# Kernel tuning notes

Measured on AMD Instinct MI355X. Metric: run time of the kernel, lower is better.

## Reference

```python
import jax, jax.numpy as jnp
import numpy as np

B, T, H, V = 64, 48, 512, 32000


def _uni(k, shape, fan_in):
    s = 1.0 / np.sqrt(fan_in)
    return jax.random.uniform(k, shape, jnp.float32, -s, s)


def setup_inputs() -> dict:
    key = jax.random.key(0)
    ks = jax.random.split(key, 21)
    inp = {
        "feat": jax.random.normal(ks[0], (B, T, H), jnp.float32),
        "caption": jax.random.normal(ks[1], (B, T, H), jnp.float32),
        "ids": jax.random.randint(ks[2], (B, T), 0, V),
    }
    i = 3
    for name, in_dim in (("1", H), ("2", 2 * H), ("d1", H), ("d2", 2 * H)):
        inp["w_ih" + name] = _uni(ks[i], (4 * H, in_dim), H); i += 1
        inp["w_hh" + name] = _uni(ks[i], (4 * H, H), H); i += 1
        inp["b_ih" + name] = _uni(ks[i], (4 * H,), H); i += 1
        inp["b_hh" + name] = _uni(ks[i], (4 * H,), H); i += 1
    inp["w_o"] = _uni(ks[i], (V, H), H); i += 1
    inp["b_o"] = _uni(ks[i], (V,), H)
    return inp


def lstm_cell(x, h, c, w_ih, w_hh, b_ih, b_hh):
    # PyTorch LSTMCell: gates in i, f, g, o order
    g = x @ w_ih.T + b_ih + h @ w_hh.T + b_hh
    gi, gf, gg, go = jnp.split(g, 4, axis=-1)
    c_new = jax.nn.sigmoid(gf) * c + jax.nn.sigmoid(gi) * jnp.tanh(gg)
    h_new = jax.nn.sigmoid(go) * jnp.tanh(c_new)
    return h_new, c_new


def reference(feat, caption, ids,
              w_ih1, w_hh1, b_ih1, b_hh1,
              w_ih2, w_hh2, b_ih2, b_hh2,
              w_ihd1, w_hhd1, b_ihd1, b_hhd1,
              w_ihd2, w_hhd2, b_ihd2, b_hhd2,
              w_o, b_o):
    pad = jnp.zeros((B, H), feat.dtype)
    z = jnp.zeros((B, H), feat.dtype)

    def enc_step(carry, x):
        h1, c1, h2, c2 = carry
        h1, c1 = lstm_cell(x, h1, c1, w_ih1, w_hh1, b_ih1, b_hh1)
        h2, c2 = lstm_cell(jnp.concatenate([pad, h1], 1), h2, c2,
                           w_ih2, w_hh2, b_ih2, b_hh2)
        return (h1, c1, h2, c2), None

    carry, _ = jax.lax.scan(enc_step, (z, z, z, z), jnp.swapaxes(feat, 0, 1))

    def dec_step(carry, xs):
        h1, c1, h2, c2 = carry
        cap, tgt = xs
        h1, c1 = lstm_cell(pad, h1, c1, w_ihd1, w_hhd1, b_ihd1, b_hhd1)
        h2, c2 = lstm_cell(jnp.concatenate([cap, h1], 1), h2, c2,
                           w_ihd2, w_hhd2, b_ihd2, b_hhd2)
        logits = h2 @ w_o.T + b_o  # [B, V]
        lp = jax.nn.log_softmax(logits, axis=-1)
        ce = -jnp.take_along_axis(lp, tgt[:, None], axis=1)[:, 0].mean()
        return (h1, c1, h2, c2), ce

    caps = jnp.swapaxes(caption[:, : T - 1, :], 0, 1)  # [T-1, B, H]
    tgts = jnp.swapaxes(ids[:, 1:T], 0, 1)             # [T-1, B]
    _, ces = jax.lax.scan(dec_step, carry, (caps, tgts))
    # total_loss += sum(mean_ce) / batch_size (word_loss is already a mean)
    return jnp.sum(ces) / B
```

## Files before the change

### kernel.cpp

```cpp
#include <hip/hip_runtime.h>
#include <math.h>

#define B_ 64
#define T_ 48
#define H_ 512
#define V_ 32000
#define G_ 2048
#define BH_ (B_*H_)
#define BG_ (B_*G_)

typedef short short8 __attribute__((ext_vector_type(8)));
typedef float f32x4 __attribute__((ext_vector_type(4)));

__device__ __forceinline__ float sigmoidf_(float x){ return 1.f/(1.f+__expf(-x)); }

__device__ __forceinline__ unsigned short f2bf(float f){
  unsigned u = __float_as_uint(f);
  u += 0x7fffu + ((u>>16)&1u);
  return (unsigned short)(u>>16);
}

__device__ __forceinline__ short8 cvt8(const float* g){
  float4 a = *(const float4*)g;
  float4 b = *(const float4*)(g+4);
  short8 v;
  v[0]=(short)f2bf(a.x); v[1]=(short)f2bf(a.y); v[2]=(short)f2bf(a.z); v[3]=(short)f2bf(a.w);
  v[4]=(short)f2bf(b.x); v[5]=(short)f2bf(b.y); v[6]=(short)f2bf(b.z); v[7]=(short)f2bf(b.w);
  return v;
}

__global__ void init_kernel(unsigned short* h1_0, unsigned short* h2_0, unsigned* flags){
  int i = blockIdx.x*256 + threadIdx.x;
  short8 z = {0,0,0,0,0,0,0,0};
  if (i < 4096) ((short8*)h1_0)[i] = z;
  else          ((short8*)h2_0)[i-4096] = z;
  if (i < 1152) flags[i] = 0u;
}

__global__ void cvt_cat_kernel(const float* __restrict__ s0, int ld0, int off0,
                               const float* __restrict__ s1, int ld1, int off1,
                               unsigned short* __restrict__ dst, int dld, long total8)
{
  int cols8 = dld >> 3;
  for (long i = blockIdx.x*256 + threadIdx.x; i < total8; i += (long)gridDim.x*256){
    int r = (int)(i / cols8);
    int k = (int)(i - (long)r*cols8) * 8;
    short8 v = (k < 512 || !s1) ? cvt8(s0 + (long)r*ld0 + off0 + k)
                                : cvt8(s1 + (long)r*ld1 + off1 + (k-512));
    *(short8*)(dst + (long)r*dld + k) = v;
  }
}

__global__ void bias_sum_kernel(const float* a1, const float* a2, float* o1,
                                const float* b1, const float* b2, float* o2){
  int n = blockIdx.x*256 + threadIdx.x;
  if (n < G_){ o1[n] = a1[n] + a2[n]; o2[n] = b1[n] + b2[n]; }
}

__global__ __launch_bounds__(512,1) void mm_pre_kernel(
    const float* __restrict__ A, int a_bstride,
    const unsigned short* __restrict__ Wbf,
    const float* __restrict__ bA, const float* __restrict__ bB,
    float* __restrict__ out)
{
  const int s = blockIdx.x, n0 = blockIdx.y*256;
  const int t = threadIdx.x, w = t>>6, l = t&63, ln = l&15, lk = l>>4;
  __shared__ short8 smA[64*64];
  __shared__ short8 smB[256*8];

  const float* af32 = A + (long)s*H_;

  f32x4 acc[4][2];
#pragma unroll
  for (int mf=0; mf<4; ++mf)
#pragma unroll
    for (int nf=0; nf<2; ++nf) acc[mf][nf] = (f32x4){0.f,0.f,0.f,0.f};

#pragma unroll
  for (int i=0;i<8;++i){ int e=i*4096+t*8; int m=e>>9, k=e&511;
    smA[m*64 + ((k>>3)^(m&7))] = cvt8(&af32[(long)m*a_bstride + k]); }

  for (int kc=0; kc<8; ++kc){
    __syncthreads();
#pragma unroll
    for (int i=0;i<4;++i){ int e=i*4096+t*8; int n=e>>6, k=e&63;
      smB[n*8 + ((k>>3)^(n&7))] = *(const short8*)(Wbf + (long)(n0+n)*512 + kc*64 + k); }
    __syncthreads();
#pragma unroll
    for (int ks2=0; ks2<2; ++ks2){
#pragma unroll
      for (int nf=0; nf<2; ++nf){
        int n = w*32 + nf*16 + ln;
        short8 bfr = smB[n*8 + ((ks2*4+lk)^(n&7))];
#pragma unroll
        for (int mf=0; mf<4; ++mf){
          int m = mf*16+ln;
          short8 afr = smA[m*64 + (((kc*2+ks2)*4+lk)^(m&7))];
          acc[mf][nf] = __builtin_amdgcn_mfma_f32_16x16x32_bf16(afr, bfr, acc[mf][nf], 0,0,0);
        }
      }
    }
  }
#pragma unroll
  for (int nf=0; nf<2; ++nf){
    int n = n0 + w*32 + nf*16 + ln;
    float bias = bA[n] + bB[n];
#pragma unroll
    for (int mf=0; mf<4; ++mf)
#pragma unroll
      for (int r=0; r<4; ++r){
        int m = mf*16 + lk*4 + r;
        out[(long)s*BG_ + (long)m*G_ + n] = acc[mf][nf][r] + bias;
      }
  }
}

__global__ __launch_bounds__(256,1) void fused_chain_kernel(
    const unsigned short* __restrict__ w1e, const unsigned short* __restrict__ w1d,
    const unsigned short* __restrict__ w2e, const unsigned short* __restrict__ w2d,
    const float* __restrict__ x1,
    const float* __restrict__ capq,
    const float* __restrict__ bd1s, const float* __restrict__ b2es,
    unsigned short* __restrict__ h1, unsigned short* __restrict__ h2,
    unsigned* __restrict__ flags)
{
  const int bc = blockIdx.x;
  const int isL2 = (bc >= 32);
  const int cb = bc & 31;
  const int t = threadIdx.x;
  const int wv = t>>6, l = t&63, ln = l&15, lk = l>>4;

  __shared__ short8 smA[64*128];
  __shared__ float gbuf[4][16][68];
  __shared__ float c_lds[16][68];
  unsigned short* stash = (unsigned short*)&smA[0];

  short8 W[32];
  const int col = wv*512 + cb*16 + ln;
  if (isL2){
    const long wrow = (long)col * 1024;
#pragma unroll
    for (int ks=0; ks<32; ++ks) W[ks] = *(const short8*)(w2e + wrow + ks*32 + lk*8);
  } else {
    const long wrow = (long)col * 512;
#pragma unroll
    for (int ks=0; ks<16; ++ks){
      W[ks]    = *(const short8*)(w1e + wrow + ks*32 + lk*8);
      W[16+ks] = *(const short8*)(w1d + wrow + ks*32 + lk*8);
    }
  }
  const float bext = isL2 ? b2es[col] : bd1s[col];

  for (int i=t; i<16*68; i+=256) (&c_lds[0][0])[i] = 0.f;

  for (int s=0; s<96; ++s){
    if (isL2 && s == 49){
      const long wrow = (long)col * 1024;
#pragma unroll
      for (int ks=0; ks<32; ++ks) W[ks] = *(const short8*)(w2d + wrow + ks*32 + lk*8);
    }
    const int active = isL2 ? (s>=1) : (s<95);
    if (active){
      if (!isL2){
        const unsigned short* hp = h1 + (long)s*BH_;
#pragma unroll
        for (int i=0;i<16;++i){ int e=i*2048+t*8; int m=e>>9, k=e&511;
          smA[m*128 + ((k>>3)^(m&7))] = *(const short8*)(hp + m*512 + k); }
      } else {
        const unsigned short* hpA = h2 + (long)(s-1)*BH_;
        const unsigned short* hpB = h1 + (long)s*BH_;
#pragma unroll
        for (int i=0;i<16;++i){ int e=i*2048+t*8; int m=e>>9, k=e&511;
          smA[m*128 + ((k>>3)^(m&7))]      = *(const short8*)(hpA + m*512 + k);
          smA[m*128 + ((k>>3)^(m&7)) + 64] = *(const short8*)(hpB + m*512 + k);
        }
      }

      const int dec = isL2 ? ((s-1)>=48) : (s>=48);
      float prev[4][4];
      if (!isL2){
        if (s < 48){
          const float* pp = x1 + (long)s*BG_ + col;
#pragma unroll
          for (int mf=0;mf<4;++mf)
#pragma unroll
            for (int r=0;r<4;++r) prev[mf][r] = pp[(long)(mf*16+lk*4+r)*G_];
        } else {
#pragma unroll
          for (int mf=0;mf<4;++mf)
#pragma unroll
            for (int r=0;r<4;++r) prev[mf][r] = bext;
        }
      } else {
        int s2 = s-1;
        if (s2 < 48){
#pragma unroll
          for (int mf=0;mf<4;++mf)
#pragma unroll
            for (int r=0;r<4;++r) prev[mf][r] = bext;
        } else {
          const float* pp = capq + (long)(s2-48)*BG_ + col;
#pragma unroll
          for (int mf=0;mf<4;++mf)
#pragma unroll
            for (int r=0;r<4;++r) prev[mf][r] = pp[(long)(mf*16+lk*4+r)*G_];
        }
      }
      __syncthreads();

      f32x4 acc[4];
#pragma unroll
      for (int mf=0;mf<4;++mf) acc[mf] = (f32x4){0.f,0.f,0.f,0.f};

      if (isL2){
#pragma unroll
        for (int ks=0; ks<32; ++ks)
#pragma unroll
          for (int mf=0; mf<4; ++mf){
            int m = mf*16+ln;
            acc[mf] = __builtin_amdgcn_mfma_f32_16x16x32_bf16(
              smA[m*128 + ((ks*4+lk)^(m&7))], W[ks], acc[mf], 0,0,0);
          }
      } else if (!dec){
#pragma unroll
        for (int ks=0; ks<16; ++ks)
#pragma unroll
          for (int mf=0; mf<4; ++mf){
            int m = mf*16+ln;
            acc[mf] = __builtin_amdgcn_mfma_f32_16x16x32_bf16(
              smA[m*128 + ((ks*4+lk)^(m&7))], W[ks], acc[mf], 0,0,0);
          }
      } else {
#pragma unroll
        for (int ks=0; ks<16; ++ks)
#pragma unroll
          for (int mf=0; mf<4; ++mf){
            int m = mf*16+ln;
            acc[mf] = __builtin_amdgcn_mfma_f32_16x16x32_bf16(
              smA[m*128 + ((ks*4+lk)^(m&7))], W[16+ks], acc[mf], 0,0,0);
          }
      }

#pragma unroll
      for (int mf=0;mf<4;++mf)
#pragma unroll
        for (int r=0;r<4;++r) acc[mf][r] += prev[mf][r];

#pragma unroll
      for (int mf=0;mf<4;++mf) *(f32x4*)&gbuf[wv][ln][mf*16+lk*4] = acc[mf];
      __syncthreads();

      {
        int n = t&15, m0 = (t>>4)*4;
        float4 gi = *(float4*)&gbuf[0][n][m0];
        float4 gf = *(float4*)&gbuf[1][n][m0];
        float4 gg = *(float4*)&gbuf[2][n][m0];
        float4 go = *(float4*)&gbuf[3][n][m0];
        float4 c4 = *(float4*)&c_lds[n][m0];
        float a_i[4]={gi.x,gi.y,gi.z,gi.w}, a_f[4]={gf.x,gf.y,gf.z,gf.w};
        float a_g[4]={gg.x,gg.y,gg.z,gg.w}, a_o[4]={go.x,go.y,go.z,go.w};
        float ci[4]={c4.x,c4.y,c4.z,c4.w};
        float cn[4];
#pragma unroll
        for (int j=0;j<4;++j){
          float i_ = sigmoidf_(a_i[j]), f_ = sigmoidf_(a_f[j]), o_ = sigmoidf_(a_o[j]);
          float g_ = tanhf(a_g[j]);
          cn[j] = f_*ci[j] + i_*g_;
          stash[(m0+j)*24 + n] = f2bf(o_*tanhf(cn[j]));
        }
        *(float4*)&c_lds[n][m0] = make_float4(cn[0],cn[1],cn[2],cn[3]);
      }
      __syncthreads();

      {
        unsigned short* ho = (isL2 ? (h2 + (long)s*BH_) : (h1 + (long)(s+1)*BH_)) + cb*16;
        int m = t>>2, q = t&3;
        unsigned long long v = *(const unsigned long long*)&stash[m*24 + q*4];
        __hip_atomic_store((unsigned long long*)(ho + (long)m*512 + q*4), v,
                           __ATOMIC_RELAXED, __HIP_MEMORY_SCOPE_AGENT);
      }
    }

    if (s < 95){
      unsigned g = (unsigned)(s+1);
      __syncthreads();
      if (t == 0)
        __hip_atomic_store(&flags[bc*16], g, __ATOMIC_RELAXED, __HIP_MEMORY_SCOPE_AGENT);
      if (t < 64){
        while (__hip_atomic_load(&flags[t*16], __ATOMIC_RELAXED, __HIP_MEMORY_SCOPE_AGENT) < g)
          __builtin_amdgcn_s_sleep(1);
      }
      __syncthreads();
    }
  }
}

__global__ __launch_bounds__(512,1) void ce_mfma_kernel(
    const unsigned short* __restrict__ h2_bf, const unsigned short* __restrict__ wo_bf,
    const float* __restrict__ b_o, const int* __restrict__ ids,
    float* __restrict__ partial, float* __restrict__ tgt)
{
  const int td = blockIdx.x, vt = blockIdx.y, v0 = vt*256;
  const int t = threadIdx.x, w = t>>6, l = t&63, ln = l&15, lk = l>>4;
  __shared__ short8 smA[64*64];
  __shared__ short8 smB[256*8];
  __shared__ float red[8][64];
  __shared__ int tid_s[64];

  const unsigned short* hp = h2_bf + (long)(49+td)*BH_;
  if (t < 64) tid_s[t] = ids[t*T_ + td + 1];
#pragma unroll
  for (int i=0;i<8;++i){ int e=i*4096+t*8; int m=e>>9, k=e&511;
    smA[m*64 + ((k>>3)^(m&7))] = *(const short8*)(hp + m*512 + k); }

  f32x4 acc[4][2];
#pragma unroll
  for (int mf=0; mf<4; ++mf)
#pragma unroll
    for (int nf=0; nf<2; ++nf) acc[mf][nf] = (f32x4){0.f,0.f,0.f,0.f};

  for (int kc=0; kc<8; ++kc){
    __syncthreads();
#pragma unroll
    for (int i=0;i<4;++i){ int e=i*4096+t*8; int n=e>>6, k=e&63;
      smB[n*8 + ((k>>3)^(n&7))] = *(const short8*)(wo_bf + (long)(v0+n)*512 + kc*64 + k); }
    __syncthreads();
#pragma unroll
    for (int ks2=0; ks2<2; ++ks2){
#pragma unroll
      for (int nf=0; nf<2; ++nf){
        int n = w*32 + nf*16 + ln;
        short8 bfr = smB[n*8 + ((ks2*4+lk)^(n&7))];
#pragma unroll
        for (int mf=0; mf<4; ++mf){
          int m = mf*16+ln;
          short8 afr = smA[m*64 + (((kc*2+ks2)*4+lk)^(m&7))];
          acc[mf][nf] = __builtin_amdgcn_mfma_f32_16x16x32_bf16(afr, bfr, acc[mf][nf], 0,0,0);
        }
      }
    }
  }

  float se[4][4];
#pragma unroll
  for (int mf=0; mf<4; ++mf)
#pragma unroll
    for (int r=0;r<4;++r) se[mf][r] = 0.f;
#pragma unroll
  for (int nf=0; nf<2; ++nf){
    int ng = v0 + w*32 + nf*16 + ln;
    float bo = b_o[ng];
#pragma unroll
    for (int mf=0; mf<4; ++mf)
#pragma unroll
      for (int r=0;r<4;++r){
        int m = mf*16 + lk*4 + r;
        float lg = acc[mf][nf][r] + bo;
        se[mf][r] += __expf(lg);
        if (ng == tid_s[m]) tgt[td*64 + m] = lg;
      }
  }
#pragma unroll
  for (int off=1; off<16; off<<=1)
#pragma unroll
    for (int mf=0; mf<4; ++mf)
#pragma unroll
      for (int r=0;r<4;++r) se[mf][r] += __shfl_xor(se[mf][r], off);
  if (ln == 0){
#pragma unroll
    for (int mf=0; mf<4; ++mf)
      *(f32x4*)&red[w][mf*16 + lk*4] = (f32x4){se[mf][0],se[mf][1],se[mf][2],se[mf][3]};
  }
  __syncthreads();
  if (t < 64){
    float ssum = 0.f;
#pragma unroll
    for (int w2=0; w2<8; ++w2) ssum += red[w2][t];
    partial[(long)vt*3008 + td*64 + t] = ssum;
  }
}

__global__ void ce_combine(const float* __restrict__ partial, const float* __restrict__ tgt,
                           float* __restrict__ ce_row){
  int r = blockIdx.x*256 + threadIdx.x;
  if (r < 3008){
    float s = 0.f;
    for (int i=0;i<125;++i) s += partial[(long)i*3008 + r];
    ce_row[r] = __logf(s) - tgt[r];
  }
}

__global__ void ce_final(const float* __restrict__ ce_row, float* __restrict__ out){
  __shared__ float red[256];
  float s = 0.f;
  for (int i=threadIdx.x; i<3008; i+=256) s += ce_row[i];
  red[threadIdx.x] = s;
  __syncthreads();
  for (int off=128; off>0; off>>=1){
    if (threadIdx.x < off) red[threadIdx.x] += red[threadIdx.x + off];
    __syncthreads();
  }
  if (threadIdx.x == 0) out[0] = red[0] * (1.0f/4096.0f);
}

extern "C" void kernel_launch(void* const* d_in, const int* in_sizes, int n_in,
                              void* d_out, int out_size, void* d_ws, size_t ws_size,
                              hipStream_t stream)
{
  (void)in_sizes; (void)n_in; (void)out_size; (void)ws_size;
  const float* feat    = (const float*)d_in[0];
  const float* caption = (const float*)d_in[1];
  const int*   ids     = (const int*)d_in[2];
  const float* w_ih1  = (const float*)d_in[3];
  const float* w_hh1  = (const float*)d_in[4];
  const float* b_ih1  = (const float*)d_in[5];
  const float* b_hh1  = (const float*)d_in[6];
  const float* w_ih2  = (const float*)d_in[7];
  const float* w_hh2  = (const float*)d_in[8];
  const float* b_ih2  = (const float*)d_in[9];
  const float* b_hh2  = (const float*)d_in[10];
  const float* w_hhd1 = (const float*)d_in[12];
  const float* b_ihd1 = (const float*)d_in[13];
  const float* b_hhd1 = (const float*)d_in[14];
  const float* w_ihd2 = (const float*)d_in[15];
  const float* w_hhd2 = (const float*)d_in[16];
  const float* b_ihd2 = (const float*)d_in[17];
  const float* b_hhd2 = (const float*)d_in[18];
  const float* w_o    = (const float*)d_in[19];
  const float* b_o    = (const float*)d_in[20];

  char* p = (char*)d_ws;
  unsigned short* h1   = (unsigned short*)p; p += 96L*BH_*2;
  unsigned short* h2   = (unsigned short*)p; p += 96L*BH_*2;
  unsigned short* w1e  = (unsigned short*)p; p += 2048L*512*2;
  unsigned short* w1d  = (unsigned short*)p; p += 2048L*512*2;
  unsigned short* w2e  = (unsigned short*)p; p += 2048L*1024*2;
  unsigned short* w2d  = (unsigned short*)p; p += 2048L*1024*2;
  unsigned short* wx1  = (unsigned short*)p; p += 2048L*512*2;
  unsigned short* wcap = (unsigned short*)p; p += 2048L*512*2;
  float* x1    = (float*)p;
  unsigned short* wo_bf = (unsigned short*)p;
  p += 48L*BG_*4;
  float* capq  = (float*)p; p += 47L*BG_*4;
  float* bd1s  = (float*)p; p += 2048*4;
  float* b2es  = (float*)p; p += 2048*4;
  float* partial = (float*)p; p += 125L*3008*4;
  float* tgt   = (float*)p; p += 3008*4;
  float* ce_row= (float*)p; p += 3008*4;
  unsigned* flags = (unsigned*)p; p += 1152*4;

  init_kernel<<<32, 256, 0, stream>>>(h1, h2, flags);

  cvt_cat_kernel<<<256, 256, 0, stream>>>(w_hh1, 512, 0, nullptr, 0, 0, w1e, 512, 2048L*64);
  cvt_cat_kernel<<<256, 256, 0, stream>>>(w_hhd1, 512, 0, nullptr, 0, 0, w1d, 512, 2048L*64);
  cvt_cat_kernel<<<256, 256, 0, stream>>>(w_hh2, 512, 0, w_ih2, 1024, 512, w2e, 1024, 2048L*128);
  cvt_cat_kernel<<<256, 256, 0, stream>>>(w_hhd2, 512, 0, w_ihd2, 1024, 512, w2d, 1024, 2048L*128);
  cvt_cat_kernel<<<256, 256, 0, stream>>>(w_ih1, 512, 0, nullptr, 0, 0, wx1, 512, 2048L*64);
  cvt_cat_kernel<<<256, 256, 0, stream>>>(w_ihd2, 1024, 0, nullptr, 0, 0, wcap, 512, 2048L*64);
  bias_sum_kernel<<<8, 256, 0, stream>>>(b_ihd1, b_hhd1, bd1s, b_ih2, b_hh2, b2es);

  mm_pre_kernel<<<dim3(48,8), 512, 0, stream>>>(feat, T_*H_, wx1, b_ih1, b_hh1, x1);
  mm_pre_kernel<<<dim3(47,8), 512, 0, stream>>>(caption, T_*H_, wcap, b_ihd2, b_hhd2, capq);

  fused_chain_kernel<<<64, 256, 0, stream>>>(w1e, w1d, w2e, w2d, x1, capq, bd1s, b2es, h1, h2, flags);

  cvt_cat_kernel<<<512, 256, 0, stream>>>(w_o, 512, 0, nullptr, 0, 0, wo_bf, 512, 32000L*64);

  ce_mfma_kernel<<<dim3(47,125), 512, 0, stream>>>(h2, wo_bf, b_o, ids, partial, tgt);
  ce_combine<<<12, 256, 0, stream>>>(partial, tgt, ce_row);
  ce_final<<<1, 256, 0, stream>>>(ce_row, (float*)d_out);
}
```

Baseline: 1.479 ms.

## Decouple layer-1 and layer-2 LSTM groups with separate counter barriers

Replaces the single 64-block all-to-all flag barrier with two independent 32-block counter/generation barriers, one per LSTM layer group. Layer-2 blocks now only wait on layer-1's generation counter, which lets layer 1 run ahead of layer 2 so the two chains pipeline instead of running in lockstep. Each barrier uses one atomic fetch_add and a single spinning thread instead of 64 threads polling 64 flags. The risks are contention on the shared counter and the need for the flags buffer to be zeroed and laid out for the new indices. Memory visibility relies only on relaxed atomics plus __syncthreads.

```diff
diff --git a/kernel.cpp b/kernel.cpp
--- a/kernel.cpp
+++ b/kernel.cpp
@@ -130,6 +130,11 @@
   const int t = threadIdx.x;
   const int wv = t>>6, l = t&63, ln = l&15, lk = l>>4;
 
+  unsigned* ctr1 = flags;
+  unsigned* gen1 = flags + 64;
+  unsigned* ctr2 = flags + 128;
+  unsigned* gen2 = flags + 192;
+
   __shared__ short8 smA[64*128];
   __shared__ float gbuf[4][16][68];
   __shared__ float c_lds[16][68];
@@ -152,76 +157,34 @@
   const float bext = isL2 ? b2es[col] : bd1s[col];
 
   for (int i=t; i<16*68; i+=256) (&c_lds[0][0])[i] = 0.f;
-
-  for (int s=0; s<96; ++s){
-    if (isL2 && s == 49){
-      const long wrow = (long)col * 1024;
-#pragma unroll
-      for (int ks=0; ks<32; ++ks) W[ks] = *(const short8*)(w2d + wrow + ks*32 + lk*8);
-    }
-    const int active = isL2 ? (s>=1) : (s<95);
-    if (active){
-      if (!isL2){
-        const unsigned short* hp = h1 + (long)s*BH_;
+  __syncthreads();
+
+  if (!isL2){
+    for (int u=0; u<95; ++u){
+      { const unsigned short* hp = h1 + (long)u*BH_;
 #pragma unroll
         for (int i=0;i<16;++i){ int e=i*2048+t*8; int m=e>>9, k=e&511;
-          smA[m*128 + ((k>>3)^(m&7))] = *(const short8*)(hp + m*512 + k); }
+          smA[m*128 + ((k>>3)^(m&7))] = *(const short8*)(hp + m*512 + k); } }
+
+      float prev[4][4];
+      if (u < 48){
+        const float* pp = x1 + (long)u*BG_ + col;
+#pragma unroll
+        for (int mf=0;mf<4;++mf)
+#pragma unroll
+          for (int r=0;r<4;++r) prev[mf][r] = pp[(long)(mf*16+lk*4+r)*G_];
       } else {
-        const unsigned short* hpA = h2 + (long)(s-1)*BH_;
-        const unsigned short* hpB = h1 + (long)s*BH_;
-#pragma unroll
-        for (int i=0;i<16;++i){ int e=i*2048+t*8; int m=e>>9, k=e&511;
-          smA[m*128 + ((k>>3)^(m&7))]      = *(const short8*)(hpA + m*512 + k);
-          smA[m*128 + ((k>>3)^(m&7)) + 64] = *(const short8*)(hpB + m*512 + k);
-        }
-      }
-
-      const int dec = isL2 ? ((s-1)>=48) : (s>=48);
-      float prev[4][4];
-      if (!isL2){
-        if (s < 48){
-          const float* pp = x1 + (long)s*BG_ + col;
-#pragma unroll
-          for (int mf=0;mf<4;++mf)
-#pragma unroll
-            for (int r=0;r<4;++r) prev[mf][r] = pp[(long)(mf*16+lk*4+r)*G_];
-        } else {
-#pragma unroll
-          for (int mf=0;mf<4;++mf)
-#pragma unroll
-            for (int r=0;r<4;++r) prev[mf][r] = bext;
-        }
-      } else {
-        int s2 = s-1;
-        if (s2 < 48){
-#pragma unroll
-          for (int mf=0;mf<4;++mf)
-#pragma unroll
-            for (int r=0;r<4;++r) prev[mf][r] = bext;
-        } else {
-          const float* pp = capq + (long)(s2-48)*BG_ + col;
-#pragma unroll
-          for (int mf=0;mf<4;++mf)
-#pragma unroll
-            for (int r=0;r<4;++r) prev[mf][r] = pp[(long)(mf*16+lk*4+r)*G_];
-        }
+#pragma unroll
+        for (int mf=0;mf<4;++mf)
+#pragma unroll
+          for (int r=0;r<4;++r) prev[mf][r] = bext;
       }
       __syncthreads();
 
       f32x4 acc[4];
 #pragma unroll
       for (int mf=0;mf<4;++mf) acc[mf] = (f32x4){0.f,0.f,0.f,0.f};
-
-      if (isL2){
-#pragma unroll
-        for (int ks=0; ks<32; ++ks)
-#pragma unroll
-          for (int mf=0; mf<4; ++mf){
-            int m = mf*16+ln;
-            acc[mf] = __builtin_amdgcn_mfma_f32_16x16x32_bf16(
-              smA[m*128 + ((ks*4+lk)^(m&7))], W[ks], acc[mf], 0,0,0);
-          }
-      } else if (!dec){
+      if (u < 48){
 #pragma unroll
         for (int ks=0; ks<16; ++ks)
 #pragma unroll
@@ -240,7 +203,6 @@
               smA[m*128 + ((ks*4+lk)^(m&7))], W[16+ks], acc[mf], 0,0,0);
           }
       }
-
 #pragma unroll
       for (int mf=0;mf<4;++mf)
 #pragma unroll
@@ -249,7 +211,6 @@
 #pragma unroll
       for (int mf=0;mf<4;++mf) *(f32x4*)&gbuf[wv][ln][mf*16+lk*4] = acc[mf];
       __syncthreads();
-
       {
         int n = t&15, m0 = (t>>4)*4;
         float4 gi = *(float4*)&gbuf[0][n][m0];
@@ -257,10 +218,10 @@
         float4 gg = *(float4*)&gbuf[2][n][m0];
         float4 go = *(float4*)&gbuf[3][n][m0];
         float4 c4 = *(float4*)&c_lds[n][m0];
+        float cn[4];
         float a_i[4]={gi.x,gi.y,gi.z,gi.w}, a_f[4]={gf.x,gf.y,gf.z,gf.w};
         float a_g[4]={gg.x,gg.y,gg.z,gg.w}, a_o[4]={go.x,go.y,go.z,go.w};
         float ci[4]={c4.x,c4.y,c4.z,c4.w};
-        float cn[4];
 #pragma unroll
         for (int j=0;j<4;++j){
           float i_ = sigmoidf_(a_i[j]), f_ = sigmoidf_(a_f[j]), o_ = sigmoidf_(a_o[j]);
@@ -271,26 +232,122 @@
         *(float4*)&c_lds[n][m0] = make_float4(cn[0],cn[1],cn[2],cn[3]);
       }
       __syncthreads();
-
       {
-        unsigned short* ho = (isL2 ? (h2 + (long)s*BH_) : (h1 + (long)(s+1)*BH_)) + cb*16;
+        unsigned short* ho = h1 + (long)(u+1)*BH_ + cb*16;
         int m = t>>2, q = t&3;
         unsigned long long v = *(const unsigned long long*)&stash[m*24 + q*4];
         __hip_atomic_store((unsigned long long*)(ho + (long)m*512 + q*4), v,
                            __ATOMIC_RELAXED, __HIP_MEMORY_SCOPE_AGENT);
       }
+      __syncthreads();
+      if (t == 0){
+        unsigned tgt = (unsigned)(u+1);
+        unsigned old = __hip_atomic_fetch_add(ctr1, 1u, __ATOMIC_RELAXED, __HIP_MEMORY_SCOPE_AGENT);
+        if (old == 32u*tgt - 1u)
+          __hip_atomic_store(gen1, tgt, __ATOMIC_RELAXED, __HIP_MEMORY_SCOPE_AGENT);
+        else
+          while (__hip_atomic_load(gen1, __ATOMIC_RELAXED, __HIP_MEMORY_SCOPE_AGENT) < tgt)
+            __builtin_amdgcn_s_sleep(1);
+      }
+      __syncthreads();
     }
-
-    if (s < 95){
-      unsigned g = (unsigned)(s+1);
-      __syncthreads();
-      if (t == 0)
-        __hip_atomic_store(&flags[bc*16], g, __ATOMIC_RELAXED, __HIP_MEMORY_SCOPE_AGENT);
-      if (t < 64){
-        while (__hip_atomic_load(&flags[t*16], __ATOMIC_RELAXED, __HIP_MEMORY_SCOPE_AGENT) < g)
+  } else {
+    for (int v=1; v<=95; ++v){
+      if (v == 49){
+        const long wrow = (long)col * 1024;
+#pragma unroll
+        for (int ks=0; ks<32; ++ks) W[ks] = *(const short8*)(w2d + wrow + ks*32 + lk*8);
+      }
+      if (t == 0){
+        while (__hip_atomic_load(gen1, __ATOMIC_RELAXED, __HIP_MEMORY_SCOPE_AGENT) < (unsigned)v)
           __builtin_amdgcn_s_sleep(1);
       }
       __syncthreads();
+
+      { const unsigned short* hpA = h2 + (long)(v-1)*BH_;
+        const unsigned short* hpB = h1 + (long)v*BH_;
+#pragma unroll
+        for (int i=0;i<16;++i){ int e=i*2048+t*8; int m=e>>9, k=e&511;
+          smA[m*128 + ((k>>3)^(m&7))]      = *(const short8*)(hpA + m*512 + k);
+          smA[m*128 + ((k>>3)^(m&7)) + 64] = *(const short8*)(hpB + m*512 + k);
+        } }
+
+      int s2 = v-1;
+      float prev[4][4];
+      if (s2 < 48){
+#pragma unroll
+        for (int mf=0;mf<4;++mf)
+#pragma unroll
+          for (int r=0;r<4;++r) prev[mf][r] = bext;
+      } else {
+        const float* pp = capq + (long)(s2-48)*BG_ + col;
+#pragma unroll
+        for (int mf=0;mf<4;++mf)
+#pragma unroll
+          for (int r=0;r<4;++r) prev[mf][r] = pp[(long)(mf*16+lk*4+r)*G_];
+      }
+      __syncthreads();
+
+      f32x4 acc[4];
+#pragma unroll
+      for (int mf=0;mf<4;++mf) acc[mf] = (f32x4){0.f,0.f,0.f,0.f};
+#pragma unroll
+      for (int ks=0; ks<32; ++ks)
+#pragma unroll
+        for (int mf=0; mf<4; ++mf){
+          int m = mf*16+ln;
+          acc[mf] = __builtin_amdgcn_mfma_f32_16x16x32_bf16(
+            smA[m*128 + ((ks*4+lk)^(m&7))], W[ks], acc[mf], 0,0,0);
+        }
+#pragma unroll
+      for (int mf=0;mf<4;++mf)
+#pragma unroll
+        for (int r=0;r<4;++r) acc[mf][r] += prev[mf][r];
+
+#pragma unroll
+      for (int mf=0;mf<4;++mf) *(f32x4*)&gbuf[wv][ln][mf*16+lk*4] = acc[mf];
+      __syncthreads();
+      {
+        int n = t&15, m0 = (t>>4)*4;
+        float4 gi = *(float4*)&gbuf[0][n][m0];
+        float4 gf = *(float4*)&gbuf[1][n][m0];
+        float4 gg = *(float4*)&gbuf[2][n][m0];
+        float4 go = *(float4*)&gbuf[3][n][m0];
+        float4 c4 = *(float4*)&c_lds[n][m0];
+        float cn[4];
+        float a_i[4]={gi.x,gi.y,gi.z,gi.w}, a_f[4]={gf.x,gf.y,gf.z,gf.w};
+        float a_g[4]={gg.x,gg.y,gg.z,gg.w}, a_o[4]={go.x,go.y,go.z,go.w};
+        float ci[4]={c4.x,c4.y,c4.z,c4.w};
+#pragma unroll
+        for (int j=0;j<4;++j){
+          float i_ = sigmoidf_(a_i[j]), f_ = sigmoidf_(a_f[j]), o_ = sigmoidf_(a_o[j]);
+          float g_ = tanhf(a_g[j]);
+          cn[j] = f_*ci[j] + i_*g_;
+          stash[(m0+j)*24 + n] = f2bf(o_*tanhf(cn[j]));
+        }
+        *(float4*)&c_lds[n][m0] = make_float4(cn[0],cn[1],cn[2],cn[3]);
+      }
+      __syncthreads();
+      {
+        unsigned short* ho = h2 + (long)v*BH_ + cb*16;
+        int m = t>>2, q = t&3;
+        unsigned long long vv = *(const unsigned long long*)&stash[m*24 + q*4];
+        __hip_atomic_store((unsigned long long*)(ho + (long)m*512 + q*4), vv,
+                           __ATOMIC_RELAXED, __HIP_MEMORY_SCOPE_AGENT);
+      }
+      __syncthreads();
+      if (v < 95){
+        if (t == 0){
+          unsigned tgt = (unsigned)v;
+          unsigned old = __hip_atomic_fetch_add(ctr2, 1u, __ATOMIC_RELAXED, __HIP_MEMORY_SCOPE_AGENT);
+          if (old == 32u*tgt - 1u)
+            __hip_atomic_store(gen2, tgt, __ATOMIC_RELAXED, __HIP_MEMORY_SCOPE_AGENT);
+          else
+            while (__hip_atomic_load(gen2, __ATOMIC_RELAXED, __HIP_MEMORY_SCOPE_AGENT) < tgt)
+              __builtin_amdgcn_s_sleep(1);
+        }
+        __syncthreads();
+      }
     }
   }
 }
```

Result: slower. 1.579 ms (+6.7%).

## Keep vocab tile resident in LDS across timesteps and store gate preacts as bf16

Applied to the files above, without the earlier changes.

The output-projection/CE kernel now launches one block per 128-wide vocab tile. Each block holds its bf16 w_o slice in shared memory and loops over all 47 decoder timesteps, streaming only the small h2 chunks. This replaces the 47x125 grid that reloaded w_o tiles from global memory for every timestep. Separately, the precomputed input-gate activations (x1, capq) are written and read as bf16 instead of fp32, halving that traffic in the serial chain kernel at some precision cost. The grid shrinks to 250 blocks with a serial timestep loop, which may limit parallelism.

```diff
diff --git a/kernel.cpp b/kernel.cpp
--- a/kernel.cpp
+++ b/kernel.cpp
@@ -18,6 +18,9 @@
   unsigned u = __float_as_uint(f);
   u += 0x7fffu + ((u>>16)&1u);
   return (unsigned short)(u>>16);
+}
+__device__ __forceinline__ float bf2f(unsigned short u){
+  return __uint_as_float(((unsigned)u)<<16);
 }
 
 __device__ __forceinline__ short8 cvt8(const float* g){
@@ -61,7 +64,7 @@
     const float* __restrict__ A, int a_bstride,
     const unsigned short* __restrict__ Wbf,
     const float* __restrict__ bA, const float* __restrict__ bB,
-    float* __restrict__ out)
+    unsigned short* __restrict__ out)
 {
   const int s = blockIdx.x, n0 = blockIdx.y*256;
   const int t = threadIdx.x, w = t>>6, l = t&63, ln = l&15, lk = l>>4;
@@ -110,7 +113,7 @@
 #pragma unroll
       for (int r=0; r<4; ++r){
         int m = mf*16 + lk*4 + r;
-        out[(long)s*BG_ + (long)m*G_ + n] = acc[mf][nf][r] + bias;
+        out[(long)s*BG_ + (long)m*G_ + n] = f2bf(acc[mf][nf][r] + bias);
       }
   }
 }
@@ -118,8 +121,8 @@
 __global__ __launch_bounds__(256,1) void fused_chain_kernel(
     const unsigned short* __restrict__ w1e, const unsigned short* __restrict__ w1d,
     const unsigned short* __restrict__ w2e, const unsigned short* __restrict__ w2d,
-    const float* __restrict__ x1,
-    const float* __restrict__ capq,
+    const unsigned short* __restrict__ x1b,
+    const unsigned short* __restrict__ capqb,
     const float* __restrict__ bd1s, const float* __restrict__ b2es,
     unsigned short* __restrict__ h1, unsigned short* __restrict__ h2,
     unsigned* __restrict__ flags)
@@ -180,11 +183,11 @@
       float prev[4][4];
       if (!isL2){
         if (s < 48){
-          const float* pp = x1 + (long)s*BG_ + col;
+          const unsigned short* pp = x1b + (long)s*BG_ + col;
 #pragma unroll
           for (int mf=0;mf<4;++mf)
 #pragma unroll
-            for (int r=0;r<4;++r) prev[mf][r] = pp[(long)(mf*16+lk*4+r)*G_];
+            for (int r=0;r<4;++r) prev[mf][r] = bf2f(pp[(long)(mf*16+lk*4+r)*G_]);
         } else {
 #pragma unroll
           for (int mf=0;mf<4;++mf)
@@ -199,11 +202,11 @@
 #pragma unroll
             for (int r=0;r<4;++r) prev[mf][r] = bext;
         } else {
-          const float* pp = capq + (long)(s2-48)*BG_ + col;
+          const unsigned short* pp = capqb + (long)(s2-48)*BG_ + col;
 #pragma unroll
           for (int mf=0;mf<4;++mf)
 #pragma unroll
-            for (int r=0;r<4;++r) prev[mf][r] = pp[(long)(mf*16+lk*4+r)*G_];
+            for (int r=0;r<4;++r) prev[mf][r] = bf2f(pp[(long)(mf*16+lk*4+r)*G_]);
         }
       }
       __syncthreads();
@@ -257,10 +260,10 @@
         float4 gg = *(float4*)&gbuf[2][n][m0];
         float4 go = *(float4*)&gbuf[3][n][m0];
         float4 c4 = *(float4*)&c_lds[n][m0];
+        float cn[4];
         float a_i[4]={gi.x,gi.y,gi.z,gi.w}, a_f[4]={gf.x,gf.y,gf.z,gf.w};
         float a_g[4]={gg.x,gg.y,gg.z,gg.w}, a_o[4]={go.x,go.y,go.z,go.w};
         float ci[4]={c4.x,c4.y,c4.z,c4.w};
-        float cn[4];
 #pragma unroll
         for (int j=0;j<4;++j){
           float i_ = sigmoidf_(a_i[j]), f_ = sigmoidf_(a_f[j]), o_ = sigmoidf_(a_o[j]);
@@ -271,7 +274,6 @@
         *(float4*)&c_lds[n][m0] = make_float4(cn[0],cn[1],cn[2],cn[3]);
       }
       __syncthreads();
-
       {
         unsigned short* ho = (isL2 ? (h2 + (long)s*BH_) : (h1 + (long)(s+1)*BH_)) + cb*16;
         int m = t>>2, q = t&3;
@@ -295,88 +297,80 @@
   }
 }
 
-__global__ __launch_bounds__(512,1) void ce_mfma_kernel(
+__global__ __launch_bounds__(512,1) void ce_vt_kernel(
     const unsigned short* __restrict__ h2_bf, const unsigned short* __restrict__ wo_bf,
     const float* __restrict__ b_o, const int* __restrict__ ids,
     float* __restrict__ partial, float* __restrict__ tgt)
 {
-  const int td = blockIdx.x, vt = blockIdx.y, v0 = vt*256;
-  const int t = threadIdx.x, w = t>>6, l = t&63, ln = l&15, lk = l>>4;
-  __shared__ short8 smA[64*64];
-  __shared__ short8 smB[256*8];
+  const int vt = blockIdx.x, v0 = vt*128;
+  const int t = threadIdx.x, wv = t>>6, l = t&63, ln = l&15, lk = l>>4;
+  __shared__ short8 smB[128*64];
+  __shared__ short8 smAc[64*8];
   __shared__ float red[8][64];
   __shared__ int tid_s[64];
 
-  const unsigned short* hp = h2_bf + (long)(49+td)*BH_;
-  if (t < 64) tid_s[t] = ids[t*T_ + td + 1];
-#pragma unroll
-  for (int i=0;i<8;++i){ int e=i*4096+t*8; int m=e>>9, k=e&511;
-    smA[m*64 + ((k>>3)^(m&7))] = *(const short8*)(hp + m*512 + k); }
-
-  f32x4 acc[4][2];
-#pragma unroll
-  for (int mf=0; mf<4; ++mf)
-#pragma unroll
-    for (int nf=0; nf<2; ++nf) acc[mf][nf] = (f32x4){0.f,0.f,0.f,0.f};
-
-  for (int kc=0; kc<8; ++kc){
-    __syncthreads();
-#pragma unroll
-    for (int i=0;i<4;++i){ int e=i*4096+t*8; int n=e>>6, k=e&63;
-      smB[n*8 + ((k>>3)^(n&7))] = *(const short8*)(wo_bf + (long)(v0+n)*512 + kc*64 + k); }
-    __syncthreads();
-#pragma unroll
-    for (int ks2=0; ks2<2; ++ks2){
-#pragma unroll
-      for (int nf=0; nf<2; ++nf){
-        int n = w*32 + nf*16 + ln;
-        short8 bfr = smB[n*8 + ((ks2*4+lk)^(n&7))];
+  for (int i = t; i < 128*64; i += 512){
+    int n = i >> 6, c = i & 63;
+    smB[n*64 + ((c & 56) | ((c & 7) ^ (n & 7)))] =
+        *(const short8*)(wo_bf + (long)(v0+n)*512 + c*8);
+  }
+  const int nn = wv*16 + ln;
+  const float bo = b_o[v0 + nn];
+  __syncthreads();
+
+  for (int td = 0; td < 47; ++td){
+    if (t < 64) tid_s[t] = ids[t*T_ + td + 1];
+    const unsigned short* hp = h2_bf + (long)(49+td)*BH_;
+
+    f32x4 acc[4];
+#pragma unroll
+    for (int mf=0;mf<4;++mf) acc[mf] = (f32x4){0.f,0.f,0.f,0.f};
+
+    for (int kc=0; kc<8; ++kc){
+      __syncthreads();
+      { int m = t>>3, c = t&7;
+        smAc[m*8 + (c ^ (m&7))] = *(const short8*)(hp + m*512 + kc*64 + c*8); }
+      __syncthreads();
+#pragma unroll
+      for (int ks2=0; ks2<2; ++ks2){
+        short8 bfr = smB[nn*64 + kc*8 + ((ks2*4+lk)^(nn&7))];
 #pragma unroll
         for (int mf=0; mf<4; ++mf){
           int m = mf*16+ln;
-          short8 afr = smA[m*64 + (((kc*2+ks2)*4+lk)^(m&7))];
-          acc[mf][nf] = __builtin_amdgcn_mfma_f32_16x16x32_bf16(afr, bfr, acc[mf][nf], 0,0,0);
-        }
-      }
-    }
-  }
-
-  float se[4][4];
-#pragma unroll
-  for (int mf=0; mf<4; ++mf)
-#pragma unroll
-    for (int r=0;r<4;++r) se[mf][r] = 0.f;
-#pragma unroll
-  for (int nf=0; nf<2; ++nf){
-    int ng = v0 + w*32 + nf*16 + ln;
-    float bo = b_o[ng];
+          short8 afr = smAc[m*8 + ((ks2*4+lk)^(m&7))];
+          acc[mf] = __builtin_amdgcn_mfma_f32_16x16x32_bf16(afr, bfr, acc[mf], 0,0,0);
+        }
+      }
+    }
+
+    float se[4][4];
 #pragma unroll
     for (int mf=0; mf<4; ++mf)
 #pragma unroll
       for (int r=0;r<4;++r){
         int m = mf*16 + lk*4 + r;
-        float lg = acc[mf][nf][r] + bo;
-        se[mf][r] += __expf(lg);
-        if (ng == tid_s[m]) tgt[td*64 + m] = lg;
-      }
-  }
-#pragma unroll
-  for (int off=1; off<16; off<<=1)
-#pragma unroll
-    for (int mf=0; mf<4; ++mf)
-#pragma unroll
-      for (int r=0;r<4;++r) se[mf][r] += __shfl_xor(se[mf][r], off);
-  if (ln == 0){
-#pragma unroll
-    for (int mf=0; mf<4; ++mf)
-      *(f32x4*)&red[w][mf*16 + lk*4] = (f32x4){se[mf][0],se[mf][1],se[mf][2],se[mf][3]};
-  }
-  __syncthreads();
-  if (t < 64){
-    float ssum = 0.f;
-#pragma unroll
-    for (int w2=0; w2<8; ++w2) ssum += red[w2][t];
-    partial[(long)vt*3008 + td*64 + t] = ssum;
+        float lg = acc[mf][r] + bo;
+        se[mf][r] = __expf(lg);
+        if (v0 + nn == tid_s[m]) tgt[td*64 + m] = lg;
+      }
+#pragma unroll
+    for (int off=1; off<16; off<<=1)
+#pragma unroll
+      for (int mf=0; mf<4; ++mf)
+#pragma unroll
+        for (int r=0;r<4;++r) se[mf][r] += __shfl_xor(se[mf][r], off);
+    if (ln == 0){
+#pragma unroll
+      for (int mf=0; mf<4; ++mf)
+        *(f32x4*)&red[wv][mf*16 + lk*4] = (f32x4){se[mf][0],se[mf][1],se[mf][2],se[mf][3]};
+    }
+    __syncthreads();
+    if (t < 64){
+      float ssum = 0.f;
+#pragma unroll
+      for (int w2=0; w2<8; ++w2) ssum += red[w2][t];
+      partial[(long)vt*3008 + td*64 + t] = ssum;
+    }
   }
 }
 
@@ -385,7 +379,7 @@
   int r = blockIdx.x*256 + threadIdx.x;
   if (r < 3008){
     float s = 0.f;
-    for (int i=0;i<125;++i) s += partial[(long)i*3008 + r];
+    for (int i=0;i<250;++i) s += partial[(long)i*3008 + r];
     ce_row[r] = __logf(s) - tgt[r];
   }
 }
@@ -430,21 +424,21 @@
   const float* b_o    = (const float*)d_in[20];
 
   char* p = (char*)d_ws;
-  unsigned short* h1   = (unsigned short*)p; p += 96L*BH_*2;
-  unsigned short* h2   = (unsigned short*)p; p += 96L*BH_*2;
-  unsigned short* w1e  = (unsigned short*)p; p += 2048L*512*2;
-  unsigned short* w1d  = (unsigned short*)p; p += 2048L*512*2;
-  unsigned short* w2e  = (unsigned short*)p; p += 2048L*1024*2;
-  unsigned short* w2d  = (unsigned short*)p; p += 2048L*1024*2;
-  unsigned short* wx1  = (unsigned short*)p; p += 2048L*512*2;
-  unsigned short* wcap = (unsigned short*)p; p += 2048L*512*2;
-  float* x1    = (float*)p;
-  unsigned short* wo_bf = (unsigned short*)p;
-  p += 48L*BG_*4;
-  float* capq  = (float*)p; p += 47L*BG_*4;
+  unsigned short* h1    = (unsigned short*)p; p += 96L*BH_*2;
+  unsigned short* h2    = (unsigned short*)p; p += 96L*BH_*2;
+  unsigned short* w2e   = (unsigned short*)p; p += 2048L*1024*2;
+  unsigned short* w2d   = (unsigned short*)p; p += 2048L*1024*2;
+  char* alias0 = p;
+  unsigned short* w1e   = (unsigned short*)p; p += 2048L*512*2;
+  unsigned short* w1d   = (unsigned short*)p; p += 2048L*512*2;
+  unsigned short* wx1   = (unsigned short*)p; p += 2048L*512*2;
+  unsigned short* wcap  = (unsigned short*)p; p += 2048L*512*2;
+  unsigned short* x1b   = (unsigned short*)p; p += 48L*BG_*2;
+  unsigned short* capqb = (unsigned short*)p; p += 47L*BG_*2;
+  unsigned short* wo_bf = (unsigned short*)alias0;
   float* bd1s  = (float*)p; p += 2048*4;
   float* b2es  = (float*)p; p += 2048*4;
-  float* partial = (float*)p; p += 125L*3008*4;
+  float* partial = (float*)p; p += 250L*3008*4;
   float* tgt   = (float*)p; p += 3008*4;
   float* ce_row= (float*)p; p += 3008*4;
   unsigned* flags = (unsigned*)p; p += 1152*4;
@@ -459,14 +453,14 @@
   cvt_cat_kernel<<<256, 256, 0, stream>>>(w_ihd2, 1024, 0, nullptr, 0, 0, wcap, 512, 2048L*64);
   bias_sum_kernel<<<8, 256, 0, stream>>>(b_ihd1, b_hhd1, bd1s, b_ih2, b_hh2, b2es);
 
-  mm_pre_kernel<<<dim3(48,8), 512, 0, stream>>>(feat, T_*H_, wx1, b_ih1, b_hh1, x1);
-  mm_pre_kernel<<<dim3(47,8), 512, 0, stream>>>(caption, T_*H_, wcap, b_ihd2, b_hhd2, capq);
-
-  fused_chain_kernel<<<64, 256, 0, stream>>>(w1e, w1d, w2e, w2d, x1, capq, bd1s, b2es, h1, h2, flags);
+  mm_pre_kernel<<<dim3(48,8), 512, 0, stream>>>(feat, T_*H_, wx1, b_ih1, b_hh1, x1b);
+  mm_pre_kernel<<<dim3(47,8), 512, 0, stream>>>(caption, T_*H_, wcap, b_ihd2, b_hhd2, capqb);
+
+  fused_chain_kernel<<<64, 256, 0, stream>>>(w1e, w1d, w2e, w2d, x1b, capqb, bd1s, b2es, h1, h2, flags);
 
   cvt_cat_kernel<<<512, 256, 0, stream>>>(w_o, 512, 0, nullptr, 0, 0, wo_bf, 512, 32000L*64);
 
-  ce_mfma_kernel<<<dim3(47,125), 512, 0, stream>>>(h2, wo_bf, b_o, ids, partial, tgt);
+  ce_vt_kernel<<<250, 512, 0, stream>>>(h2, wo_bf, b_o, ids, partial, tgt);
   ce_combine<<<12, 256, 0, stream>>>(partial, tgt, ce_row);
   ce_final<<<1, 256, 0, stream>>>(ce_row, (float*)d_out);
 }
```

Result: slower. 1.580 ms (+6.8%).
